# Optimization experiments

Hardware: AMD Instinct MI355X
Metric: run time of the kernel (lower is better)

## Reference

```python
import jax, jax.numpy as jnp
import numpy as np

BATCH = 32768
HIDDEN = 512
OUT = 2
FUTURE_STEPS = 60


def _lstm_cell(x, h, c, w_ih, w_hh, b_ih, b_hh):
    # PyTorch gate order: i, f, g, o
    g = x @ w_ih.T + h @ w_hh.T + b_ih + b_hh
    i, f, gg, o = jnp.split(g, 4, axis=-1)
    c_new = jax.nn.sigmoid(f) * c + jax.nn.sigmoid(i) * jnp.tanh(gg)
    h_new = jax.nn.sigmoid(o) * jnp.tanh(c_new)
    return h_new, c_new


def setup_inputs() -> dict:
    key = jax.random.key(0)
    ks = jax.random.split(key, 16)
    s = 0.05
    inp = {
        "h": jax.random.normal(ks[0], (BATCH, HIDDEN), jnp.float32),
        "w_init_h": jax.random.normal(ks[1], (HIDDEN, HIDDEN), jnp.float32) * s,
        "b_init_h": jax.random.normal(ks[2], (HIDDEN,), jnp.float32) * s,
        "w_init_c": jax.random.normal(ks[3], (HIDDEN, HIDDEN), jnp.float32) * s,
        "b_init_c": jax.random.normal(ks[4], (HIDDEN,), jnp.float32) * s,
        "w_ih0": jax.random.normal(ks[5], (4 * HIDDEN, OUT), jnp.float32) * s,
        "w_hh0": jax.random.normal(ks[6], (4 * HIDDEN, HIDDEN), jnp.float32) * s,
        "b_ih0": jax.random.normal(ks[7], (4 * HIDDEN,), jnp.float32) * s,
        "b_hh0": jax.random.normal(ks[8], (4 * HIDDEN,), jnp.float32) * s,
        "w_ih1": jax.random.normal(ks[9], (4 * HIDDEN, HIDDEN), jnp.float32) * s,
        "w_hh1": jax.random.normal(ks[10], (4 * HIDDEN, HIDDEN), jnp.float32) * s,
        "b_ih1": jax.random.normal(ks[11], (4 * HIDDEN,), jnp.float32) * s,
        "b_hh1": jax.random.normal(ks[12], (4 * HIDDEN,), jnp.float32) * s,
        "w_out": jax.random.normal(ks[13], (OUT, HIDDEN), jnp.float32) * s,
        "b_out": jax.random.normal(ks[14], (OUT,), jnp.float32) * s,
    }
    return inp


def reference(h, w_init_h, b_init_h, w_init_c, b_init_c,
              w_ih0, w_hh0, b_ih0, b_hh0,
              w_ih1, w_hh1, b_ih1, b_hh1,
              w_out, b_out):
    batch = h.shape[0]
    # same initial (h, c) replicated to both LSTM layers (repeat(2,1,1))
    h0 = h @ w_init_h.T + b_init_h
    c0 = h @ w_init_c.T + b_init_c
    x0 = jnp.zeros((batch, OUT), h.dtype)

    def step(carry, _):
        x, h1, c1, h2, c2 = carry
        h1, c1 = _lstm_cell(x, h1, c1, w_ih0, w_hh0, b_ih0, b_hh0)
        h2, c2 = _lstm_cell(h1, h2, c2, w_ih1, w_hh1, b_ih1, b_hh1)
        pred = h2 @ w_out.T + b_out  # [batch, OUT]
        return (pred, h1, c1, h2, c2), pred

    _, preds = jax.lax.scan(step, (x0, h0, c0, h0, c0), None, length=FUTURE_STEPS)
    return jnp.transpose(preds, (1, 0, 2))  # [batch, future_steps, OUT]
```

## Files before the change

kernel.cpp:

```cpp
#include <hip/hip_runtime.h>

#define HID    512
#define TPB    512
#define NSTEP  60
#define BMI    64

using f32x4 = __attribute__((ext_vector_type(4))) float;
using s16x8 = __attribute__((ext_vector_type(8))) short;

__device__ __forceinline__ unsigned short f2bf(float f) {
    unsigned u = __builtin_bit_cast(unsigned, f);
    u += 0x7fffu + ((u >> 16) & 1u);
    return (unsigned short)(u >> 16);
}
__device__ __forceinline__ float bf2f(unsigned u) {
    return __builtin_bit_cast(float, u << 16);
}
__device__ __forceinline__ float sigm(float x) { return 1.0f / (1.0f + __expf(-x)); }
__device__ __forceinline__ float tanh_(float x) { return 1.0f - 2.0f / (__expf(2.0f * x) + 1.0f); }

__global__ void pack_kernel(const float* __restrict__ w_hh0, const float* __restrict__ w_ih1,
                            const float* __restrict__ w_hh1, const float* __restrict__ w_init_h,
                            const float* __restrict__ w_init_c,
                            const float* __restrict__ b_ih0, const float* __restrict__ b_hh0,
                            const float* __restrict__ b_ih1, const float* __restrict__ b_hh1,
                            unsigned short* __restrict__ PW1, unsigned short* __restrict__ PW2,
                            unsigned short* __restrict__ PI,
                            float* __restrict__ b1, float* __restrict__ b2)
{
    int idx = blockIdx.x * 256 + threadIdx.x;
    if (idx < 1048576) {
        int el = idx & 511, fr = idx >> 9;
        int ks = fr & 15, ct = (fr >> 4) & 7, s = fr >> 7;
        int lane = el >> 3, e = el & 7;
        int l15 = lane & 15;
        int gcol = (l15 & 3) * 512 + s * 32 + ct * 4 + (l15 >> 2);
        int k = ks * 32 + (lane >> 4) * 8 + e;
        PW1[idx] = f2bf(w_hh0[gcol * 512 + k]);
        return;
    }
    int i2 = idx - 1048576;
    if (i2 >= 0 && i2 < 2097152) {
        int el = i2 & 511, fr = i2 >> 9;
        int ks = fr & 31, ct = (fr >> 5) & 7, s = fr >> 8;
        int lane = el >> 3, e = el & 7;
        int l15 = lane & 15;
        int gcol = (l15 & 3) * 512 + s * 32 + ct * 4 + (l15 >> 2);
        int kk = (ks & 15) * 32 + (lane >> 4) * 8 + e;
        float v = (ks < 16) ? w_ih1[gcol * 512 + kk] : w_hh1[gcol * 512 + kk];
        PW2[i2] = f2bf(v);
        return;
    }
    int i3 = idx - (1048576 + 2097152);
    if (i3 >= 0 && i3 < 524288) {
        int el = i3 & 511, fr = i3 >> 9;
        int ks = fr & 15, tile = fr >> 4;
        int s = tile >> 5, c = tile & 31;
        int lane = el >> 3, e = el & 7;
        int n = c * 16 + (lane & 15);
        int k = ks * 32 + (lane >> 4) * 8 + e;
        float v = s ? w_init_c[n * 512 + k] : w_init_h[n * 512 + k];
        PI[i3] = f2bf(v);
        return;
    }
    int i4 = idx - (1048576 + 2097152 + 524288);
    if (i4 >= 0 && i4 < 2048) b1[i4] = b_ih0[i4] + b_hh0[i4];
    else if (i4 >= 2048 && i4 < 4096) b2[i4 - 2048] = b_ih1[i4 - 2048] + b_hh1[i4 - 2048];
}

__global__ __launch_bounds__(TPB, 2) void init_kernel(
    const float* __restrict__ hin, const unsigned short* __restrict__ PI,
    const float* __restrict__ b_init_h, const float* __restrict__ b_init_c,
    unsigned short* __restrict__ h1s, unsigned short* __restrict__ h2s,
    unsigned short* __restrict__ c1s, unsigned short* __restrict__ c2s)
{
    __shared__ unsigned short bufA[BMI * HID];
    const int tid = threadIdx.x, lane = tid & 63, wave = tid >> 6;
    const int m0 = blockIdx.x * BMI;
    const int l15 = lane & 15, lg = lane >> 4;
    const int swz = (lane & 7) << 4;

    for (int j = 0; j < 16; ++j) {
        int e = tid * 4 + j * 2048;
        int row = e >> 9, col = e & 511;
        float4 v = *(const float4*)(hin + (size_t)(m0 + row) * HID + col);
        ushort4 w;
        w.x = f2bf(v.x); w.y = f2bf(v.y); w.z = f2bf(v.z); w.w = f2bf(v.w);
        int L = (row * 1024 + col * 2) ^ ((row & 7) << 4);
        *(ushort4*)((char*)bufA + L) = w;
    }
    __syncthreads();

    #pragma unroll 1
    for (int cc = 0; cc < 4; ++cc) {
        int c = wave * 4 + cc;
        int nc = c * 16 + l15;
        f32x4 acc[4][2];
        #pragma unroll
        for (int rt = 0; rt < 4; ++rt)
            #pragma unroll
            for (int s = 0; s < 2; ++s)
                #pragma unroll
                for (int r = 0; r < 4; ++r) acc[rt][s][r] = 0.0f;

        #pragma unroll
        for (int ks = 0; ks < 16; ++ks) {
            s16x8 a[4];
            #pragma unroll
            for (int rt = 0; rt < 4; ++rt) {
                int ao = (rt * 16 + l15) * 1024 + ((ks * 64 + lg * 16) ^ swz);
                a[rt] = *(const s16x8*)((const char*)bufA + ao);
            }
            #pragma unroll
            for (int s = 0; s < 2; ++s) {
                s16x8 b = ((const s16x8*)PI)[((s * 32 + c) * 16 + ks) * 64 + lane];
                #pragma unroll
                for (int rt = 0; rt < 4; ++rt)
                    acc[rt][s] = __builtin_amdgcn_mfma_f32_16x16x32_bf16(a[rt], b, acc[rt][s], 0, 0, 0);
            }
        }
        float bh = b_init_h[nc], bc = b_init_c[nc];
        #pragma unroll
        for (int rt = 0; rt < 4; ++rt)
            #pragma unroll
            for (int r = 0; r < 4; ++r) {
                int m = m0 + rt * 16 + lg * 4 + r;
                float hv = acc[rt][0][r] + bh;
                float cv = acc[rt][1][r] + bc;
                unsigned short hb = f2bf(hv);
                size_t o = (size_t)m * HID + nc;
                h1s[o] = hb; h2s[o] = hb;
                c1s[o] = f2bf(cv); c2s[o] = f2bf(cv);
            }
    }
}

__global__ __launch_bounds__(TPB, 2) void l1_kernel(
    const unsigned short* __restrict__ h1R, unsigned short* __restrict__ h1W,
    unsigned short* __restrict__ c1s, const float* __restrict__ pp,
    float* __restrict__ outp, const unsigned short* __restrict__ PW1,
    const float* __restrict__ b1, const float* __restrict__ w_ih0,
    const float* __restrict__ b_out, int t)
{
    __shared__ __align__(16) unsigned short Ab[16384];
    __shared__ __align__(16) float glf[2 * 4224];
    __shared__ __align__(16) float xls[4096];

    const int tid = threadIdx.x, lane = tid & 63, w = tid >> 6;
    const int b = blockIdx.x;
    const int g = 2 * (b & 7) + (b >> 7);
    const int s = (b >> 3) & 15;
    const int m0 = g * 2048;
    const int l15 = lane & 15, lg = lane >> 4;
    const int cg = w >> 1, kh = w & 1;

    s16x8 bw[2][8];
    #pragma unroll
    for (int j = 0; j < 2; ++j)
        #pragma unroll
        for (int ksl = 0; ksl < 8; ++ksl)
            bw[j][ksl] = ((const s16x8*)PW1)[(((s * 8 + cg * 2 + j) * 16) + kh * 8 + ksl) * 64 + lane];

    const int erow = tid >> 4, ejp = tid & 15;
    float b1v[8], wiA[8], wiB[8];
    #pragma unroll
    for (int q = 0; q < 8; ++q) {
        int dj = q & 1, gq = q >> 1;
        int gcol = gq * 512 + s * 32 + ejp * 2 + dj;
        b1v[q] = b1[gcol];
        wiA[q] = w_ih0[gcol * 2 + 0];
        wiB[q] = w_ih0[gcol * 2 + 1];
    }
    float bo0 = b_out[0], bo1 = b_out[1];

    if (t == 0) {
        #pragma unroll
        for (int i = 0; i < 8; ++i) xls[tid * 8 + i] = 0.0f;
    } else {
        f32x4 s0 = {0.f,0.f,0.f,0.f}, s1 = {0.f,0.f,0.f,0.f};
        #pragma unroll 1
        for (int ss = 0; ss < 16; ++ss) {
            const float* p = pp + (((size_t)(g * 16 + ss)) << 12) + tid * 8;
            s0 += *(const f32x4*)p;
            s1 += *(const f32x4*)(p + 4);
        }
        s0[0] += bo0; s0[1] += bo1; s0[2] += bo0; s0[3] += bo1;
        s1[0] += bo0; s1[1] += bo1; s1[2] += bo0; s1[3] += bo1;
        *(f32x4*)(xls + tid * 8) = s0;
        *(f32x4*)(xls + tid * 8 + 4) = s1;
        if (s == 0) {
            float* ob = outp + (size_t)(m0 + tid * 4) * (2 * NSTEP) + (t - 1) * 2;
            *(float2*)(ob)             = make_float2(s0[0], s0[1]);
            *(float2*)(ob + 2 * NSTEP) = make_float2(s0[2], s0[3]);
            *(float2*)(ob + 4 * NSTEP) = make_float2(s1[0], s1[1]);
            *(float2*)(ob + 6 * NSTEP) = make_float2(s1[2], s1[3]);
        }
    }

    const int st_l15 = tid & 15, st_lg = (tid >> 4) & 3, st_rh = (tid >> 6) & 1, st_kq = tid >> 7;
    const int st_grow = st_rh * 16 + st_l15;

    uint4 nv[4];
    #pragma unroll
    for (int p = 0; p < 4; ++p) {
        int ks = p * 4 + st_kq;
        uint4 v = *(const uint4*)(h1R + (size_t)(m0 + st_grow) * HID + ks * 32 + st_lg * 8);
        *(uint4*)((char*)Ab + p * 8192 + tid * 16) = v;
    }
    #pragma unroll
    for (int p = 0; p < 4; ++p) {
        int ks = p * 4 + st_kq;
        nv[p] = *(const uint4*)(h1R + (size_t)(m0 + 32 + st_grow) * HID + ks * 32 + st_lg * 8);
    }
    unsigned cpr = *(const unsigned*)(c1s + (size_t)(m0 + erow) * HID + s * 32 + ejp * 2);
    __syncthreads();

    #pragma unroll 1
    for (int ch = 0; ch < 64; ++ch) {
        f32x4 acc[2][2];
        #pragma unroll
        for (int j = 0; j < 2; ++j)
            #pragma unroll
            for (int rh = 0; rh < 2; ++rh) { acc[j][rh][0]=0.f; acc[j][rh][1]=0.f; acc[j][rh][2]=0.f; acc[j][rh][3]=0.f; }
        #pragma unroll
        for (int ksl = 0; ksl < 8; ++ksl) {
            int ks = kh * 8 + ksl;
            s16x8 a0 = *(const s16x8*)((const char*)Ab + ks * 2048 + lane * 16);
            s16x8 a1 = *(const s16x8*)((const char*)Ab + ks * 2048 + 1024 + lane * 16);
            #pragma unroll
            for (int j = 0; j < 2; ++j) {
                acc[j][0] = __builtin_amdgcn_mfma_f32_16x16x32_bf16(a0, bw[j][ksl], acc[j][0], 0, 0, 0);
                acc[j][1] = __builtin_amdgcn_mfma_f32_16x16x32_bf16(a1, bw[j][ksl], acc[j][1], 0, 0, 0);
            }
        }
        #pragma unroll
        for (int j = 0; j < 2; ++j) {
            int col = (cg * 2 + j) * 16 + l15;
            #pragma unroll
            for (int rh = 0; rh < 2; ++rh)
                #pragma unroll
                for (int r = 0; r < 4; ++r)
                    glf[kh * 4224 + (rh * 16 + lg * 4 + r) * 132 + col] = acc[j][rh][r];
        }
        __syncthreads();

        if (ch < 63) {
            #pragma unroll
            for (int p = 0; p < 4; ++p)
                *(uint4*)((char*)Ab + p * 8192 + tid * 16) = nv[p];
        }
        if (ch < 62) {
            #pragma unroll
            for (int p = 0; p < 4; ++p) {
                int ks = p * 4 + st_kq;
                nv[p] = *(const uint4*)(h1R + (size_t)(m0 + (ch + 2) * 32 + st_grow) * HID + ks * 32 + st_lg * 8);
            }
        }
        unsigned cnx = 0;
        if (ch < 63)
            cnx = *(const unsigned*)(c1s + (size_t)(m0 + (ch + 1) * 32 + erow) * HID + s * 32 + ejp * 2);

        {
            int grow = ch * 32 + erow;
            int m = m0 + grow;
            float x0 = xls[grow * 2 + 0], x1 = xls[grow * 2 + 1];
            int gbase = erow * 132 + ejp * 8;
            f32x4 qa = *(const f32x4*)&glf[gbase];
            qa += *(const f32x4*)&glf[4224 + gbase];
            f32x4 qb = *(const f32x4*)&glf[gbase + 4];
            qb += *(const f32x4*)&glf[4224 + gbase + 4];

            float cold0 = bf2f(cpr & 0xffffu), cold1 = bf2f(cpr >> 16);
            float i0 = sigm(qa[0] + b1v[0] + x0 * wiA[0] + x1 * wiB[0]);
            float f0 = sigm(qa[1] + b1v[2] + x0 * wiA[2] + x1 * wiB[2]);
            float g0 = tanh_(qa[2] + b1v[4] + x0 * wiA[4] + x1 * wiB[4]);
            float o0 = sigm(qa[3] + b1v[6] + x0 * wiA[6] + x1 * wiB[6]);
            float cn0 = f0 * cold0 + i0 * g0;
            float hn0 = o0 * tanh_(cn0);
            float i1 = sigm(qb[0] + b1v[1] + x0 * wiA[1] + x1 * wiB[1]);
            float f1 = sigm(qb[1] + b1v[3] + x0 * wiA[3] + x1 * wiB[3]);
            float g1 = tanh_(qb[2] + b1v[5] + x0 * wiA[5] + x1 * wiB[5]);
            float o1 = sigm(qb[3] + b1v[7] + x0 * wiA[7] + x1 * wiB[7]);
            float cn1 = f1 * cold1 + i1 * g1;
            float hn1 = o1 * tanh_(cn1);
            size_t cix = (size_t)m * HID + s * 32 + ejp * 2;
            *(unsigned*)(c1s + cix) = (unsigned)f2bf(cn0) | ((unsigned)f2bf(cn1) << 16);
            *(unsigned*)(h1W + cix) = (unsigned)f2bf(hn0) | ((unsigned)f2bf(hn1) << 16);
        }
        cpr = cnx;
        __syncthreads();
    }
}

__global__ __launch_bounds__(TPB, 2) void l2_kernel(
    const unsigned short* __restrict__ h1C, const unsigned short* __restrict__ h2R,
    unsigned short* __restrict__ h2W, unsigned short* __restrict__ c2s,
    float* __restrict__ pp,
    const unsigned short* __restrict__ PW2, const float* __restrict__ b2,
    const float* __restrict__ w_out)
{
    __shared__ __align__(16) unsigned short Ab[32768];
    __shared__ __align__(16) float glf[2 * 4224];

    const int tid = threadIdx.x, lane = tid & 63, w = tid >> 6;
    const int b = blockIdx.x;
    const int g = 2 * (b & 7) + (b >> 7);
    const int s = (b >> 3) & 15;
    const int m0 = g * 2048;
    const int l15 = lane & 15, lg = lane >> 4;
    const int cg = w >> 1, kh = w & 1;

    s16x8 bw[2][16];
    #pragma unroll
    for (int j = 0; j < 2; ++j)
        #pragma unroll
        for (int ksl = 0; ksl < 16; ++ksl)
            bw[j][ksl] = ((const s16x8*)PW2)[(((s * 8 + cg * 2 + j) * 32) + kh * 16 + ksl) * 64 + lane];

    const int erow = tid >> 4, ejp = tid & 15;
    float b2v[8];
    #pragma unroll
    for (int q = 0; q < 8; ++q) {
        int dj = q & 1, gq = q >> 1;
        b2v[q] = b2[gq * 512 + s * 32 + ejp * 2 + dj];
    }
    float woA0 = w_out[s * 32 + ejp * 2], woA1 = w_out[s * 32 + ejp * 2 + 1];
    float woB0 = w_out[512 + s * 32 + ejp * 2], woB1 = w_out[512 + s * 32 + ejp * 2 + 1];

    const int st_l15 = tid & 15, st_lg = (tid >> 4) & 3, st_rh = (tid >> 6) & 1, st_kq = tid >> 7;
    const int st_grow = st_rh * 16 + st_l15;

    uint4 nv[8];
    #pragma unroll
    for (int p = 0; p < 8; ++p) {
        int ks = p * 4 + st_kq;
        const unsigned short* src = (ks < 16) ? h1C : h2R;
        int kel = (ks < 16) ? ks : (ks - 16);
        uint4 v = *(const uint4*)(src + (size_t)(m0 + st_grow) * HID + kel * 32 + st_lg * 8);
        *(uint4*)((char*)Ab + p * 8192 + tid * 16) = v;
    }
    #pragma unroll
    for (int p = 0; p < 8; ++p) {
        int ks = p * 4 + st_kq;
        const unsigned short* src = (ks < 16) ? h1C : h2R;
        int kel = (ks < 16) ? ks : (ks - 16);
        nv[p] = *(const uint4*)(src + (size_t)(m0 + 32 + st_grow) * HID + kel * 32 + st_lg * 8);
    }
    unsigned cpr = *(const unsigned*)(c2s + (size_t)(m0 + erow) * HID + s * 32 + ejp * 2);
    __syncthreads();

    #pragma unroll 1
    for (int ch = 0; ch < 64; ++ch) {
        f32x4 acc[2][2];
        #pragma unroll
        for (int j = 0; j < 2; ++j)
            #pragma unroll
            for (int rh = 0; rh < 2; ++rh) { acc[j][rh][0]=0.f; acc[j][rh][1]=0.f; acc[j][rh][2]=0.f; acc[j][rh][3]=0.f; }
        #pragma unroll
        for (int ksl = 0; ksl < 16; ++ksl) {
            int ks = kh * 16 + ksl;
            s16x8 a0 = *(const s16x8*)((const char*)Ab + ks * 2048 + lane * 16);
            s16x8 a1 = *(const s16x8*)((const char*)Ab + ks * 2048 + 1024 + lane * 16);
            #pragma unroll
            for (int j = 0; j < 2; ++j) {
                acc[j][0] = __builtin_amdgcn_mfma_f32_16x16x32_bf16(a0, bw[j][ksl], acc[j][0], 0, 0, 0);
                acc[j][1] = __builtin_amdgcn_mfma_f32_16x16x32_bf16(a1, bw[j][ksl], acc[j][1], 0, 0, 0);
            }
        }
        #pragma unroll
        for (int j = 0; j < 2; ++j) {
            int col = (cg * 2 + j) * 16 + l15;
            #pragma unroll
            for (int rh = 0; rh < 2; ++rh)
                #pragma unroll
                for (int r = 0; r < 4; ++r)
                    glf[kh * 4224 + (rh * 16 + lg * 4 + r) * 132 + col] = acc[j][rh][r];
        }
        __syncthreads();

        if (ch < 63) {
            #pragma unroll
            for (int p = 0; p < 8; ++p)
                *(uint4*)((char*)Ab + p * 8192 + tid * 16) = nv[p];
        }
        if (ch < 62) {
            #pragma unroll
            for (int p = 0; p < 8; ++p) {
                int ks = p * 4 + st_kq;
                const unsigned short* src = (ks < 16) ? h1C : h2R;
                int kel = (ks < 16) ? ks : (ks - 16);
                nv[p] = *(const uint4*)(src + (size_t)(m0 + (ch + 2) * 32 + st_grow) * HID + kel * 32 + st_lg * 8);
            }
        }
        unsigned cnx = 0;
        if (ch < 63)
            cnx = *(const unsigned*)(c2s + (size_t)(m0 + (ch + 1) * 32 + erow) * HID + s * 32 + ejp * 2);

        {
            int grow = ch * 32 + erow;
            int m = m0 + grow;
            int gbase = erow * 132 + ejp * 8;
            f32x4 qa = *(const f32x4*)&glf[gbase];
            qa += *(const f32x4*)&glf[4224 + gbase];
            f32x4 qb = *(const f32x4*)&glf[gbase + 4];
            qb += *(const f32x4*)&glf[4224 + gbase + 4];

            float cold0 = bf2f(cpr & 0xffffu), cold1 = bf2f(cpr >> 16);
            float i0 = sigm(qa[0] + b2v[0]);
            float f0 = sigm(qa[1] + b2v[2]);
            float g0 = tanh_(qa[2] + b2v[4]);
            float o0 = sigm(qa[3] + b2v[6]);
            float cn0 = f0 * cold0 + i0 * g0;
            float hn0 = o0 * tanh_(cn0);
            float i1 = sigm(qb[0] + b2v[1]);
            float f1 = sigm(qb[1] + b2v[3]);
            float g1 = tanh_(qb[2] + b2v[5]);
            float o1 = sigm(qb[3] + b2v[7]);
            float cn1 = f1 * cold1 + i1 * g1;
            float hn1 = o1 * tanh_(cn1);
            size_t cix = (size_t)m * HID + s * 32 + ejp * 2;
            *(unsigned*)(c2s + cix) = (unsigned)f2bf(cn0) | ((unsigned)f2bf(cn1) << 16);
            *(unsigned*)(h2W + cix) = (unsigned)f2bf(hn0) | ((unsigned)f2bf(hn1) << 16);

            float p0 = hn0 * woA0 + hn1 * woA1;
            float p1 = hn0 * woB0 + hn1 * woB1;
            #pragma unroll
            for (int d = 1; d < 16; d <<= 1) {
                p0 += __shfl_xor(p0, d, 16);
                p1 += __shfl_xor(p1, d, 16);
            }
            if (ejp == 0)
                *(float2*)(pp + (((size_t)(g * 16 + s)) << 12) + (size_t)grow * 2)
                    = make_float2(p0, p1);
        }
        cpr = cnx;
        __syncthreads();
    }
}

__global__ void tail_kernel(const float* __restrict__ pp, const float* __restrict__ b_out,
                            float* __restrict__ outp)
{
    int i = blockIdx.x * 256 + threadIdx.x;
    if (i < 65536) {
        int m = i >> 1, j = i & 1;
        int g = m >> 11;
        int idx = (m & 2047) * 2 + j;
        float sum = b_out[j];
        #pragma unroll 1
        for (int s = 0; s < 16; ++s)
            sum += pp[(((size_t)(g * 16 + s)) << 12) + idx];
        outp[(size_t)m * (2 * NSTEP) + (NSTEP - 1) * 2 + j] = sum;
    }
}

extern "C" void kernel_launch(void* const* d_in, const int* in_sizes, int n_in,
                              void* d_out, int out_size, void* d_ws, size_t ws_size,
                              hipStream_t stream)
{
    (void)in_sizes; (void)n_in; (void)out_size; (void)ws_size;
    const float* h        = (const float*)d_in[0];
    const float* w_init_h = (const float*)d_in[1];
    const float* b_init_h = (const float*)d_in[2];
    const float* w_init_c = (const float*)d_in[3];
    const float* b_init_c = (const float*)d_in[4];
    const float* w_ih0    = (const float*)d_in[5];
    const float* w_hh0    = (const float*)d_in[6];
    const float* b_ih0    = (const float*)d_in[7];
    const float* b_hh0    = (const float*)d_in[8];
    const float* w_ih1    = (const float*)d_in[9];
    const float* w_hh1    = (const float*)d_in[10];
    const float* b_ih1    = (const float*)d_in[11];
    const float* b_hh1    = (const float*)d_in[12];
    const float* w_out    = (const float*)d_in[13];
    const float* b_out    = (const float*)d_in[14];
    float* out = (float*)d_out;

    char* ws = (char*)d_ws;
    unsigned short* h1s[2] = { (unsigned short*)(ws + 0),
                               (unsigned short*)(ws + 33554432) };
    unsigned short* h2s[2] = { (unsigned short*)(ws + 67108864),
                               (unsigned short*)(ws + 100663296) };
    unsigned short* c1s = (unsigned short*)(ws + 134217728);
    unsigned short* c2s = (unsigned short*)(ws + 167772160);
    float* pp           = (float*)(ws + 201326592);
    unsigned short* PW1 = (unsigned short*)(ws + 205520896);
    unsigned short* PW2 = (unsigned short*)(ws + 207618048);
    unsigned short* PI  = (unsigned short*)(ws + 211812352);
    float* b1 = (float*)(ws + 212860928);
    float* b2 = (float*)(ws + 212869120);

    pack_kernel<<<14352, 256, 0, stream>>>(w_hh0, w_ih1, w_hh1, w_init_h, w_init_c,
                                           b_ih0, b_hh0, b_ih1, b_hh1, PW1, PW2, PI, b1, b2);
    init_kernel<<<32768 / BMI, TPB, 0, stream>>>(h, PI, b_init_h, b_init_c,
                                                 h1s[1], h2s[1], c1s, c2s);
    for (int t = 0; t < NSTEP; ++t) {
        const unsigned short* h1R = h1s[(t + 1) & 1];
        unsigned short* h1W = h1s[t & 1];
        const unsigned short* h2R = h2s[(t + 1) & 1];
        unsigned short* h2W = h2s[t & 1];
        l1_kernel<<<256, TPB, 0, stream>>>(h1R, h1W, c1s, pp, out, PW1, b1, w_ih0, b_out, t);
        l2_kernel<<<256, TPB, 0, stream>>>(h1W, h2R, h2W, c2s, pp, PW2, b2, w_out);
    }
    tail_kernel<<<256, 256, 0, stream>>>(pp, b_out, out);
}
```

Measured before the change: 37.85 ms.

## Double threads per block in LSTM step kernels, one output column per thread

Raises the l1/l2 step kernels from 512 to 1024 threads per block. Each wave now computes a single 16-column tile instead of two, and each epilogue thread handles one hidden unit instead of a pair. The goal is more waves per CU to hide latency and to halve per-wave register pressure from the preloaded weight fragments. The cost is twice as many waves reaching each barrier, 16-bit scalar global stores instead of packed 32-bit ones, and a wider shuffle reduction for the output projection.

New measurement: 35.89 ms. 5.2% less time.

```diff
diff --git a/kernel.cpp b/kernel.cpp
--- a/kernel.cpp
+++ b/kernel.cpp
@@ -2,6 +2,7 @@
 
 #define HID    512
 #define TPB    512
+#define TPB2   1024
 #define NSTEP  60
 #define BMI    64
 
@@ -135,7 +136,7 @@
     }
 }
 
-__global__ __launch_bounds__(TPB, 2) void l1_kernel(
+__global__ __launch_bounds__(TPB2, 4) void l1_kernel(
     const unsigned short* __restrict__ h1R, unsigned short* __restrict__ h1W,
     unsigned short* __restrict__ c1s, const float* __restrict__ pp,
     float* __restrict__ outp, const unsigned short* __restrict__ PW1,
@@ -152,147 +153,121 @@
     const int s = (b >> 3) & 15;
     const int m0 = g * 2048;
     const int l15 = lane & 15, lg = lane >> 4;
-    const int cg = w >> 1, kh = w & 1;
-
-    s16x8 bw[2][8];
-    #pragma unroll
-    for (int j = 0; j < 2; ++j)
-        #pragma unroll
-        for (int ksl = 0; ksl < 8; ++ksl)
-            bw[j][ksl] = ((const s16x8*)PW1)[(((s * 8 + cg * 2 + j) * 16) + kh * 8 + ksl) * 64 + lane];
-
-    const int erow = tid >> 4, ejp = tid & 15;
-    float b1v[8], wiA[8], wiB[8];
-    #pragma unroll
-    for (int q = 0; q < 8; ++q) {
-        int dj = q & 1, gq = q >> 1;
-        int gcol = gq * 512 + s * 32 + ejp * 2 + dj;
-        b1v[q] = b1[gcol];
-        wiA[q] = w_ih0[gcol * 2 + 0];
-        wiB[q] = w_ih0[gcol * 2 + 1];
+    const int ct = w & 7, kh = w >> 3;
+
+    s16x8 bw[8];
+    #pragma unroll
+    for (int ksl = 0; ksl < 8; ++ksl)
+        bw[ksl] = ((const s16x8*)PW1)[(((s * 8 + ct) * 16) + kh * 8 + ksl) * 64 + lane];
+
+    const int erow = tid >> 5, eu = tid & 31;
+    float b1v[4], wiA[4], wiB[4];
+    #pragma unroll
+    for (int k = 0; k < 4; ++k) {
+        int gcol = k * 512 + s * 32 + eu;
+        b1v[k] = b1[gcol];
+        wiA[k] = w_ih0[gcol * 2 + 0];
+        wiB[k] = w_ih0[gcol * 2 + 1];
     }
     float bo0 = b_out[0], bo1 = b_out[1];
 
     if (t == 0) {
         #pragma unroll
-        for (int i = 0; i < 8; ++i) xls[tid * 8 + i] = 0.0f;
+        for (int i = 0; i < 4; ++i) xls[tid * 4 + i] = 0.0f;
     } else {
-        f32x4 s0 = {0.f,0.f,0.f,0.f}, s1 = {0.f,0.f,0.f,0.f};
+        f32x4 s0 = {0.f,0.f,0.f,0.f};
         #pragma unroll 1
-        for (int ss = 0; ss < 16; ++ss) {
-            const float* p = pp + (((size_t)(g * 16 + ss)) << 12) + tid * 8;
-            s0 += *(const f32x4*)p;
-            s1 += *(const f32x4*)(p + 4);
-        }
+        for (int ss = 0; ss < 16; ++ss)
+            s0 += *(const f32x4*)(pp + (((size_t)(g * 16 + ss)) << 12) + tid * 4);
         s0[0] += bo0; s0[1] += bo1; s0[2] += bo0; s0[3] += bo1;
-        s1[0] += bo0; s1[1] += bo1; s1[2] += bo0; s1[3] += bo1;
-        *(f32x4*)(xls + tid * 8) = s0;
-        *(f32x4*)(xls + tid * 8 + 4) = s1;
+        *(f32x4*)(xls + tid * 4) = s0;
         if (s == 0) {
-            float* ob = outp + (size_t)(m0 + tid * 4) * (2 * NSTEP) + (t - 1) * 2;
+            float* ob = outp + (size_t)(m0 + tid * 2) * (2 * NSTEP) + (t - 1) * 2;
             *(float2*)(ob)             = make_float2(s0[0], s0[1]);
             *(float2*)(ob + 2 * NSTEP) = make_float2(s0[2], s0[3]);
-            *(float2*)(ob + 4 * NSTEP) = make_float2(s1[0], s1[1]);
-            *(float2*)(ob + 6 * NSTEP) = make_float2(s1[2], s1[3]);
-        }
-    }
-
-    const int st_l15 = tid & 15, st_lg = (tid >> 4) & 3, st_rh = (tid >> 6) & 1, st_kq = tid >> 7;
+        }
+    }
+
+    const int st_l15 = tid & 15, st_lg = (tid >> 4) & 3, st_rh = (tid >> 6) & 1, st_kb = tid >> 7;
     const int st_grow = st_rh * 16 + st_l15;
 
-    uint4 nv[4];
-    #pragma unroll
-    for (int p = 0; p < 4; ++p) {
-        int ks = p * 4 + st_kq;
+    uint4 nv[2];
+    #pragma unroll
+    for (int p = 0; p < 2; ++p) {
+        int ks = p * 8 + st_kb;
         uint4 v = *(const uint4*)(h1R + (size_t)(m0 + st_grow) * HID + ks * 32 + st_lg * 8);
-        *(uint4*)((char*)Ab + p * 8192 + tid * 16) = v;
-    }
-    #pragma unroll
-    for (int p = 0; p < 4; ++p) {
-        int ks = p * 4 + st_kq;
+        *(uint4*)((char*)Ab + p * 16384 + tid * 16) = v;
+    }
+    #pragma unroll
+    for (int p = 0; p < 2; ++p) {
+        int ks = p * 8 + st_kb;
         nv[p] = *(const uint4*)(h1R + (size_t)(m0 + 32 + st_grow) * HID + ks * 32 + st_lg * 8);
     }
-    unsigned cpr = *(const unsigned*)(c1s + (size_t)(m0 + erow) * HID + s * 32 + ejp * 2);
+    unsigned short cpr = c1s[(size_t)(m0 + erow) * HID + s * 32 + eu];
     __syncthreads();
 
     #pragma unroll 1
     for (int ch = 0; ch < 64; ++ch) {
-        f32x4 acc[2][2];
-        #pragma unroll
-        for (int j = 0; j < 2; ++j)
-            #pragma unroll
-            for (int rh = 0; rh < 2; ++rh) { acc[j][rh][0]=0.f; acc[j][rh][1]=0.f; acc[j][rh][2]=0.f; acc[j][rh][3]=0.f; }
+        f32x4 acc[2];
+        acc[0][0]=0.f; acc[0][1]=0.f; acc[0][2]=0.f; acc[0][3]=0.f;
+        acc[1][0]=0.f; acc[1][1]=0.f; acc[1][2]=0.f; acc[1][3]=0.f;
         #pragma unroll
         for (int ksl = 0; ksl < 8; ++ksl) {
             int ks = kh * 8 + ksl;
             s16x8 a0 = *(const s16x8*)((const char*)Ab + ks * 2048 + lane * 16);
             s16x8 a1 = *(const s16x8*)((const char*)Ab + ks * 2048 + 1024 + lane * 16);
-            #pragma unroll
-            for (int j = 0; j < 2; ++j) {
-                acc[j][0] = __builtin_amdgcn_mfma_f32_16x16x32_bf16(a0, bw[j][ksl], acc[j][0], 0, 0, 0);
-                acc[j][1] = __builtin_amdgcn_mfma_f32_16x16x32_bf16(a1, bw[j][ksl], acc[j][1], 0, 0, 0);
-            }
-        }
-        #pragma unroll
-        for (int j = 0; j < 2; ++j) {
-            int col = (cg * 2 + j) * 16 + l15;
+            acc[0] = __builtin_amdgcn_mfma_f32_16x16x32_bf16(a0, bw[ksl], acc[0], 0, 0, 0);
+            acc[1] = __builtin_amdgcn_mfma_f32_16x16x32_bf16(a1, bw[ksl], acc[1], 0, 0, 0);
+        }
+        {
+            int col = ct * 16 + l15;
             #pragma unroll
             for (int rh = 0; rh < 2; ++rh)
                 #pragma unroll
                 for (int r = 0; r < 4; ++r)
-                    glf[kh * 4224 + (rh * 16 + lg * 4 + r) * 132 + col] = acc[j][rh][r];
+                    glf[kh * 4224 + (rh * 16 + lg * 4 + r) * 132 + col] = acc[rh][r];
         }
         __syncthreads();
 
         if (ch < 63) {
             #pragma unroll
-            for (int p = 0; p < 4; ++p)
-                *(uint4*)((char*)Ab + p * 8192 + tid * 16) = nv[p];
+            for (int p = 0; p < 2; ++p)
+                *(uint4*)((char*)Ab + p * 16384 + tid * 16) = nv[p];
         }
         if (ch < 62) {
             #pragma unroll
-            for (int p = 0; p < 4; ++p) {
-                int ks = p * 4 + st_kq;
+            for (int p = 0; p < 2; ++p) {
+                int ks = p * 8 + st_kb;
                 nv[p] = *(const uint4*)(h1R + (size_t)(m0 + (ch + 2) * 32 + st_grow) * HID + ks * 32 + st_lg * 8);
             }
         }
-        unsigned cnx = 0;
+        unsigned short cnx = 0;
         if (ch < 63)
-            cnx = *(const unsigned*)(c1s + (size_t)(m0 + (ch + 1) * 32 + erow) * HID + s * 32 + ejp * 2);
+            cnx = c1s[(size_t)(m0 + (ch + 1) * 32 + erow) * HID + s * 32 + eu];
 
         {
             int grow = ch * 32 + erow;
-            int m = m0 + grow;
             float x0 = xls[grow * 2 + 0], x1 = xls[grow * 2 + 1];
-            int gbase = erow * 132 + ejp * 8;
-            f32x4 qa = *(const f32x4*)&glf[gbase];
-            qa += *(const f32x4*)&glf[4224 + gbase];
-            f32x4 qb = *(const f32x4*)&glf[gbase + 4];
-            qb += *(const f32x4*)&glf[4224 + gbase + 4];
-
-            float cold0 = bf2f(cpr & 0xffffu), cold1 = bf2f(cpr >> 16);
-            float i0 = sigm(qa[0] + b1v[0] + x0 * wiA[0] + x1 * wiB[0]);
-            float f0 = sigm(qa[1] + b1v[2] + x0 * wiA[2] + x1 * wiB[2]);
-            float g0 = tanh_(qa[2] + b1v[4] + x0 * wiA[4] + x1 * wiB[4]);
-            float o0 = sigm(qa[3] + b1v[6] + x0 * wiA[6] + x1 * wiB[6]);
-            float cn0 = f0 * cold0 + i0 * g0;
-            float hn0 = o0 * tanh_(cn0);
-            float i1 = sigm(qb[0] + b1v[1] + x0 * wiA[1] + x1 * wiB[1]);
-            float f1 = sigm(qb[1] + b1v[3] + x0 * wiA[3] + x1 * wiB[3]);
-            float g1 = tanh_(qb[2] + b1v[5] + x0 * wiA[5] + x1 * wiB[5]);
-            float o1 = sigm(qb[3] + b1v[7] + x0 * wiA[7] + x1 * wiB[7]);
-            float cn1 = f1 * cold1 + i1 * g1;
-            float hn1 = o1 * tanh_(cn1);
-            size_t cix = (size_t)m * HID + s * 32 + ejp * 2;
-            *(unsigned*)(c1s + cix) = (unsigned)f2bf(cn0) | ((unsigned)f2bf(cn1) << 16);
-            *(unsigned*)(h1W + cix) = (unsigned)f2bf(hn0) | ((unsigned)f2bf(hn1) << 16);
+            int base = erow * 132 + (eu >> 2) * 16 + (eu & 3) * 4;
+            f32x4 q = *(const f32x4*)&glf[base];
+            q += *(const f32x4*)&glf[4224 + base];
+            float iv = sigm(q[0] + b1v[0] + x0 * wiA[0] + x1 * wiB[0]);
+            float fv = sigm(q[1] + b1v[1] + x0 * wiA[1] + x1 * wiB[1]);
+            float gv = tanh_(q[2] + b1v[2] + x0 * wiA[2] + x1 * wiB[2]);
+            float ov = sigm(q[3] + b1v[3] + x0 * wiA[3] + x1 * wiB[3]);
+            float cold = bf2f(cpr);
+            float cn = fv * cold + iv * gv;
+            float hn = ov * tanh_(cn);
+            size_t cix = (size_t)(m0 + grow) * HID + s * 32 + eu;
+            c1s[cix] = f2bf(cn);
+            h1W[cix] = f2bf(hn);
         }
         cpr = cnx;
         __syncthreads();
     }
 }
 
-__global__ __launch_bounds__(TPB, 2) void l2_kernel(
+__global__ __launch_bounds__(TPB2, 4) void l2_kernel(
     const unsigned short* __restrict__ h1C, const unsigned short* __restrict__ h2R,
     unsigned short* __restrict__ h2W, unsigned short* __restrict__ c2s,
     float* __restrict__ pp,
@@ -308,128 +283,105 @@
     const int s = (b >> 3) & 15;
     const int m0 = g * 2048;
     const int l15 = lane & 15, lg = lane >> 4;
-    const int cg = w >> 1, kh = w & 1;
-
-    s16x8 bw[2][16];
-    #pragma unroll
-    for (int j = 0; j < 2; ++j)
-        #pragma unroll
-        for (int ksl = 0; ksl < 16; ++ksl)
-            bw[j][ksl] = ((const s16x8*)PW2)[(((s * 8 + cg * 2 + j) * 32) + kh * 16 + ksl) * 64 + lane];
-
-    const int erow = tid >> 4, ejp = tid & 15;
-    float b2v[8];
-    #pragma unroll
-    for (int q = 0; q < 8; ++q) {
-        int dj = q & 1, gq = q >> 1;
-        b2v[q] = b2[gq * 512 + s * 32 + ejp * 2 + dj];
-    }
-    float woA0 = w_out[s * 32 + ejp * 2], woA1 = w_out[s * 32 + ejp * 2 + 1];
-    float woB0 = w_out[512 + s * 32 + ejp * 2], woB1 = w_out[512 + s * 32 + ejp * 2 + 1];
-
-    const int st_l15 = tid & 15, st_lg = (tid >> 4) & 3, st_rh = (tid >> 6) & 1, st_kq = tid >> 7;
+    const int ct = w & 7, kh = w >> 3;
+
+    s16x8 bw[16];
+    #pragma unroll
+    for (int ksl = 0; ksl < 16; ++ksl)
+        bw[ksl] = ((const s16x8*)PW2)[(((s * 8 + ct) * 32) + kh * 16 + ksl) * 64 + lane];
+
+    const int erow = tid >> 5, eu = tid & 31;
+    float b2v[4];
+    #pragma unroll
+    for (int k = 0; k < 4; ++k) b2v[k] = b2[k * 512 + s * 32 + eu];
+    const float wo0 = w_out[s * 32 + eu], wo1 = w_out[512 + s * 32 + eu];
+
+    const int st_l15 = tid & 15, st_lg = (tid >> 4) & 3, st_rh = (tid >> 6) & 1, st_kb = tid >> 7;
     const int st_grow = st_rh * 16 + st_l15;
 
-    uint4 nv[8];
-    #pragma unroll
-    for (int p = 0; p < 8; ++p) {
-        int ks = p * 4 + st_kq;
+    uint4 nv[4];
+    #pragma unroll
+    for (int p = 0; p < 4; ++p) {
+        int ks = p * 8 + st_kb;
         const unsigned short* src = (ks < 16) ? h1C : h2R;
         int kel = (ks < 16) ? ks : (ks - 16);
         uint4 v = *(const uint4*)(src + (size_t)(m0 + st_grow) * HID + kel * 32 + st_lg * 8);
-        *(uint4*)((char*)Ab + p * 8192 + tid * 16) = v;
-    }
-    #pragma unroll
-    for (int p = 0; p < 8; ++p) {
-        int ks = p * 4 + st_kq;
+        *(uint4*)((char*)Ab + p * 16384 + tid * 16) = v;
+    }
+    #pragma unroll
+    for (int p = 0; p < 4; ++p) {
+        int ks = p * 8 + st_kb;
         const unsigned short* src = (ks < 16) ? h1C : h2R;
         int kel = (ks < 16) ? ks : (ks - 16);
         nv[p] = *(const uint4*)(src + (size_t)(m0 + 32 + st_grow) * HID + kel * 32 + st_lg * 8);
     }
-    unsigned cpr = *(const unsigned*)(c2s + (size_t)(m0 + erow) * HID + s * 32 + ejp * 2);
+    unsigned short cpr = c2s[(size_t)(m0 + erow) * HID + s * 32 + eu];
     __syncthreads();
 
     #pragma unroll 1
     for (int ch = 0; ch < 64; ++ch) {
-        f32x4 acc[2][2];
-        #pragma unroll
-        for (int j = 0; j < 2; ++j)
-            #pragma unroll
-            for (int rh = 0; rh < 2; ++rh) { acc[j][rh][0]=0.f; acc[j][rh][1]=0.f; acc[j][rh][2]=0.f; acc[j][rh][3]=0.f; }
+        f32x4 acc[2];
+        acc[0][0]=0.f; acc[0][1]=0.f; acc[0][2]=0.f; acc[0][3]=0.f;
+        acc[1][0]=0.f; acc[1][1]=0.f; acc[1][2]=0.f; acc[1][3]=0.f;
         #pragma unroll
         for (int ksl = 0; ksl < 16; ++ksl) {
             int ks = kh * 16 + ksl;
             s16x8 a0 = *(const s16x8*)((const char*)Ab + ks * 2048 + lane * 16);
             s16x8 a1 = *(const s16x8*)((const char*)Ab + ks * 2048 + 1024 + lane * 16);
-            #pragma unroll
-            for (int j = 0; j < 2; ++j) {
-                acc[j][0] = __builtin_amdgcn_mfma_f32_16x16x32_bf16(a0, bw[j][ksl], acc[j][0], 0, 0, 0);
-                acc[j][1] = __builtin_amdgcn_mfma_f32_16x16x32_bf16(a1, bw[j][ksl], acc[j][1], 0, 0, 0);
-            }
-        }
-        #pragma unroll
-        for (int j = 0; j < 2; ++j) {
-            int col = (cg * 2 + j) * 16 + l15;
+            acc[0] = __builtin_amdgcn_mfma_f32_16x16x32_bf16(a0, bw[ksl], acc[0], 0, 0, 0);
+            acc[1] = __builtin_amdgcn_mfma_f32_16x16x32_bf16(a1, bw[ksl], acc[1], 0, 0, 0);
+        }
+        {
+            int col = ct * 16 + l15;
             #pragma unroll
             for (int rh = 0; rh < 2; ++rh)
                 #pragma unroll
                 for (int r = 0; r < 4; ++r)
-                    glf[kh * 4224 + (rh * 16 + lg * 4 + r) * 132 + col] = acc[j][rh][r];
+                    glf[kh * 4224 + (rh * 16 + lg * 4 + r) * 132 + col] = acc[rh][r];
         }
         __syncthreads();
 
         if (ch < 63) {
             #pragma unroll
-            for (int p = 0; p < 8; ++p)
-                *(uint4*)((char*)Ab + p * 8192 + tid * 16) = nv[p];
+            for (int p = 0; p < 4; ++p)
+                *(uint4*)((char*)Ab + p * 16384 + tid * 16) = nv[p];
         }
         if (ch < 62) {
             #pragma unroll
-            for (int p = 0; p < 8; ++p) {
-                int ks = p * 4 + st_kq;
+            for (int p = 0; p < 4; ++p) {
+                int ks = p * 8 + st_kb;
                 const unsigned short* src = (ks < 16) ? h1C : h2R;
                 int kel = (ks < 16) ? ks : (ks - 16);
                 nv[p] = *(const uint4*)(src + (size_t)(m0 + (ch + 2) * 32 + st_grow) * HID + kel * 32 + st_lg * 8);
             }
         }
-        unsigned cnx = 0;
+        unsigned short cnx = 0;
         if (ch < 63)
-            cnx = *(const unsigned*)(c2s + (size_t)(m0 + (ch + 1) * 32 + erow) * HID + s * 32 + ejp * 2);
+            cnx = c2s[(size_t)(m0 + (ch + 1) * 32 + erow) * HID + s * 32 + eu];
 
         {
             int grow = ch * 32 + erow;
-            int m = m0 + grow;
-            int gbase = erow * 132 + ejp * 8;
-            f32x4 qa = *(const f32x4*)&glf[gbase];
-            qa += *(const f32x4*)&glf[4224 + gbase];
-            f32x4 qb = *(const f32x4*)&glf[gbase + 4];
-            qb += *(const f32x4*)&glf[4224 + gbase + 4];
-
-            float cold0 = bf2f(cpr & 0xffffu), cold1 = bf2f(cpr >> 16);
-            float i0 = sigm(qa[0] + b2v[0]);
-            float f0 = sigm(qa[1] + b2v[2]);
-            float g0 = tanh_(qa[2] + b2v[4]);
-            float o0 = sigm(qa[3] + b2v[6]);
-            float cn0 = f0 * cold0 + i0 * g0;
-            float hn0 = o0 * tanh_(cn0);
-            float i1 = sigm(qb[0] + b2v[1]);
-            float f1 = sigm(qb[1] + b2v[3]);
-            float g1 = tanh_(qb[2] + b2v[5]);
-            float o1 = sigm(qb[3] + b2v[7]);
-            float cn1 = f1 * cold1 + i1 * g1;
-            float hn1 = o1 * tanh_(cn1);
-            size_t cix = (size_t)m * HID + s * 32 + ejp * 2;
-            *(unsigned*)(c2s + cix) = (unsigned)f2bf(cn0) | ((unsigned)f2bf(cn1) << 16);
-            *(unsigned*)(h2W + cix) = (unsigned)f2bf(hn0) | ((unsigned)f2bf(hn1) << 16);
-
-            float p0 = hn0 * woA0 + hn1 * woA1;
-            float p1 = hn0 * woB0 + hn1 * woB1;
-            #pragma unroll
-            for (int d = 1; d < 16; d <<= 1) {
-                p0 += __shfl_xor(p0, d, 16);
-                p1 += __shfl_xor(p1, d, 16);
-            }
-            if (ejp == 0)
+            int base = erow * 132 + (eu >> 2) * 16 + (eu & 3) * 4;
+            f32x4 q = *(const f32x4*)&glf[base];
+            q += *(const f32x4*)&glf[4224 + base];
+            float iv = sigm(q[0] + b2v[0]);
+            float fv = sigm(q[1] + b2v[1]);
+            float gv = tanh_(q[2] + b2v[2]);
+            float ov = sigm(q[3] + b2v[3]);
+            float cold = bf2f(cpr);
+            float cn = fv * cold + iv * gv;
+            float hn = ov * tanh_(cn);
+            size_t cix = (size_t)(m0 + grow) * HID + s * 32 + eu;
+            c2s[cix] = f2bf(cn);
+            h2W[cix] = f2bf(hn);
+
+            float p0 = hn * wo0, p1 = hn * wo1;
+            #pragma unroll
+            for (int d = 1; d < 32; d <<= 1) {
+                p0 += __shfl_xor(p0, d, 32);
+                p1 += __shfl_xor(p1, d, 32);
+            }
+            if (eu == 0)
                 *(float2*)(pp + (((size_t)(g * 16 + s)) << 12) + (size_t)grow * 2)
                     = make_float2(p0, p1);
         }
@@ -499,8 +451,8 @@
         unsigned short* h1W = h1s[t & 1];
         const unsigned short* h2R = h2s[(t + 1) & 1];
         unsigned short* h2W = h2s[t & 1];
-        l1_kernel<<<256, TPB, 0, stream>>>(h1R, h1W, c1s, pp, out, PW1, b1, w_ih0, b_out, t);
-        l2_kernel<<<256, TPB, 0, stream>>>(h1W, h2R, h2W, c2s, pp, PW2, b2, w_out);
+        l1_kernel<<<256, TPB2, 0, stream>>>(h1R, h1W, c1s, pp, out, PW1, b1, w_ih0, b_out, t);
+        l2_kernel<<<256, TPB2, 0, stream>>>(h1W, h2R, h2W, c2s, pp, PW2, b2, w_out);
     }
     tail_kernel<<<256, 256, 0, stream>>>(pp, b_out, out);
 }
```
